# Performance work log

Measured on AMD Instinct MI355X. Metric: run time of the kernel, lower is better.

The kernel has to match this reference:

```python
import jax, jax.numpy as jnp
import numpy as np

N = 8192
TAU = 0.5
B = 4096


def _factorize(n, tau):
    # Precompute LU factorization of the tridiagonal implicit-Laplace matrix,
    # mirroring the torch __init__ exactly.
    b = np.full(n - 1, -tau, dtype=np.float32)   # upper diagonal
    a = np.full(n, 1.0 + 2.0 * tau, dtype=np.float32)  # main diagonal
    c = np.full(n - 1, -tau, dtype=np.float32)   # lower diagonal
    a[0] = 1.0 + tau
    a[-1] = 1.0 + tau
    for i in range(n - 1):
        c[i] = c[i] / a[i]
        a[i + 1] = a[i + 1] - c[i] * b[i]
    return a, b, c


def setup_inputs() -> dict:
    key = jax.random.key(0)
    a, b, c = _factorize(N, TAU)
    x = jax.random.normal(key, (B, N), dtype=jnp.float32)
    return {
        "x": x,
        "a": jnp.asarray(a),
        "b": jnp.asarray(b),
        "c": jnp.asarray(c),
    }


def reference(x, a, b, c):
    # Thomas algorithm with precomputed LU factors.
    # Forward substitution:  y[0] = x[0];  y[i] = x[i] - y[i-1] * c[i-1]
    # Back substitution:     z[N-1] = y[N-1] / a[N-1];
    #                        z[i]   = (y[i] - z[i+1] * b[i]) / a[i]
    xt = x.T  # [N, B] so the scan runs over the grid axis
    c_pad = jnp.concatenate([jnp.zeros((1,), x.dtype), c])  # c_pad[0]=0 -> y[0]=x[0]

    def fwd_step(y_prev, inp):
        xi, ci = inp
        yi = xi - y_prev * ci
        return yi, yi

    _, y = jax.lax.scan(fwd_step, jnp.zeros_like(xt[0]), (xt, c_pad))

    b_pad = jnp.concatenate([b, jnp.zeros((1,), x.dtype)])  # b_pad[N-1]=0

    def bwd_step(z_next, inp):
        yi, bi, ai = inp
        zi = (yi - z_next * bi) / ai
        return zi, zi

    _, z = jax.lax.scan(bwd_step, jnp.zeros_like(y[0]), (y, b_pad, a), reverse=True)
    return z.T  # [B, N]
```

## Files before the change

kernel.cpp:

```cpp
#include <hip/hip_runtime.h>


#define NN    8192
#define BB    4096
#define CHUNK 128
#define HALO  32
#define WIN   (CHUNK + HALO)

__device__ __forceinline__ float fast_rcp(float v) {
#if defined(__has_builtin) && __has_builtin(__builtin_amdgcn_rcpf)
    float r = __builtin_amdgcn_rcpf(v);
    r = r * (2.0f - v * r);
    return r;
#else
    return 1.0f / v;
#endif
}

template<bool FIRST, bool EDGE>
__device__ __forceinline__ void solve_window(
    const float* __restrict__ xrow,
    const float* __restrict__ a,
    const float* __restrict__ b,
    const float* __restrict__ c,
    float* __restrict__ orow,
    int s)
{
    const float* xs = xrow + s;
    const float* as = a + s;
    const float* bs = b + s;
    const float* cs = c + s;

    float y = 0.0f;

    if (!FIRST) {
        const float* xw = xrow + (s - HALO);
        const float* cw = c + (s - HALO);
        #pragma unroll
        for (int k = 0; k < HALO; k += 4) {
            float4 xv = *(const float4*)(xw + k);
            y = xv.x - cw[k - 1] * y;
            y = xv.y - cw[k]     * y;
            y = xv.z - cw[k + 1] * y;
            y = xv.w - cw[k + 2] * y;
        }
    }

    float ybuf[WIN];
    #pragma unroll
    for (int k = 0; k < (EDGE ? CHUNK : WIN); k += 4) {
        float4 xv = *(const float4*)(xs + k);
        float c0 = (FIRST && k == 0) ? 0.0f : cs[k - 1];
        y = xv.x - c0        * y;  ybuf[k]     = y;
        y = xv.y - cs[k]     * y;  ybuf[k + 1] = y;
        y = xv.z - cs[k + 1] * y;  ybuf[k + 2] = y;
        y = xv.w - cs[k + 2] * y;  ybuf[k + 3] = y;
    }

    float z = 0.0f;
    if (!EDGE) {
        #pragma unroll
        for (int k = WIN - 1; k >= CHUNK; --k) {
            z = (ybuf[k] - bs[k] * z) * fast_rcp(as[k]);
        }
        #pragma unroll
        for (int kg = CHUNK - 4; kg >= 0; kg -= 4) {
            float4 zv;
            z = (ybuf[kg + 3] - bs[kg + 3] * z) * fast_rcp(as[kg + 3]); zv.w = z;
            z = (ybuf[kg + 2] - bs[kg + 2] * z) * fast_rcp(as[kg + 2]); zv.z = z;
            z = (ybuf[kg + 1] - bs[kg + 1] * z) * fast_rcp(as[kg + 1]); zv.y = z;
            z = (ybuf[kg]     - bs[kg]     * z) * fast_rcp(as[kg]);     zv.x = z;
            *(float4*)(orow + s + kg) = zv;
        }
    } else {
        {
            float4 zv;
            z = ybuf[CHUNK - 1] * fast_rcp(as[CHUNK - 1]);                          zv.w = z;
            z = (ybuf[CHUNK - 2] - bs[CHUNK - 2] * z) * fast_rcp(as[CHUNK - 2]);    zv.z = z;
            z = (ybuf[CHUNK - 3] - bs[CHUNK - 3] * z) * fast_rcp(as[CHUNK - 3]);    zv.y = z;
            z = (ybuf[CHUNK - 4] - bs[CHUNK - 4] * z) * fast_rcp(as[CHUNK - 4]);    zv.x = z;
            *(float4*)(orow + s + CHUNK - 4) = zv;
        }
        #pragma unroll
        for (int kg = CHUNK - 8; kg >= 0; kg -= 4) {
            float4 zv;
            z = (ybuf[kg + 3] - bs[kg + 3] * z) * fast_rcp(as[kg + 3]); zv.w = z;
            z = (ybuf[kg + 2] - bs[kg + 2] * z) * fast_rcp(as[kg + 2]); zv.z = z;
            z = (ybuf[kg + 1] - bs[kg + 1] * z) * fast_rcp(as[kg + 1]); zv.y = z;
            z = (ybuf[kg]     - bs[kg]     * z) * fast_rcp(as[kg]);     zv.x = z;
            *(float4*)(orow + s + kg) = zv;
        }
    }
}

__global__ __launch_bounds__(256, 2) void TriDiagonalLaplaceSolver_kernel(
    const float* __restrict__ x,
    const float* __restrict__ a,
    const float* __restrict__ b,
    const float* __restrict__ c,
    float* __restrict__ out)
{
    const int chunk = blockIdx.x;
    const int row   = blockIdx.y * 256 + threadIdx.x;
    const int s     = chunk * CHUNK;

    const float* xrow = x   + (size_t)row * NN;
    float*       orow = out + (size_t)row * NN;

    if (chunk == 0) {
        solve_window<true, false>(xrow, a, b, c, orow, 0);
    } else if (chunk == (NN / CHUNK) - 1) {
        solve_window<false, true>(xrow, a, b, c, orow, s);
    } else {
        solve_window<false, false>(xrow, a, b, c, orow, s);
    }
}

extern "C" void kernel_launch(void* const* d_in, const int* in_sizes, int n_in,
                              void* d_out, int out_size, void* d_ws, size_t ws_size,
                              hipStream_t stream) {
    const float* x = (const float*)d_in[0];
    const float* a = (const float*)d_in[1];
    const float* b = (const float*)d_in[2];
    const float* c = (const float*)d_in[3];
    float* out = (float*)d_out;

    dim3 grid(NN / CHUNK, BB / 256);
    dim3 block(256);
    TriDiagonalLaplaceSolver_kernel<<<grid, block, 0, stream>>>(x, a, b, c, out);
}
```

Before: 316.3 us.

## Halve chunk size, raise occupancy, and defer output stores until after back-substitution

Shrinks each thread's chunk from 128 to 64 elements and raises the launch-bounds minimum from 2 to 4 blocks per CU, so the smaller register buffer allows more waves in flight. Back-substitution now writes results into the register buffer, and all float4 stores happen in a final loop instead of being interleaved with the recurrence. The cost is more redundant halo work, since 32 extra elements per 64 outputs is a larger share than before, and more grid blocks. The preprocessor fallback around the rcp builtin is also removed.

```diff
diff --git a/kernel.cpp b/kernel.cpp
--- a/kernel.cpp
+++ b/kernel.cpp
@@ -3,18 +3,14 @@
 
 #define NN    8192
 #define BB    4096
-#define CHUNK 128
+#define CHUNK 64
 #define HALO  32
 #define WIN   (CHUNK + HALO)
 
 __device__ __forceinline__ float fast_rcp(float v) {
-#if defined(__has_builtin) && __has_builtin(__builtin_amdgcn_rcpf)
     float r = __builtin_amdgcn_rcpf(v);
     r = r * (2.0f - v * r);
     return r;
-#else
-    return 1.0f / v;
-#endif
 }
 
 template<bool FIRST, bool EDGE>
@@ -64,36 +60,32 @@
             z = (ybuf[k] - bs[k] * z) * fast_rcp(as[k]);
         }
         #pragma unroll
-        for (int kg = CHUNK - 4; kg >= 0; kg -= 4) {
-            float4 zv;
-            z = (ybuf[kg + 3] - bs[kg + 3] * z) * fast_rcp(as[kg + 3]); zv.w = z;
-            z = (ybuf[kg + 2] - bs[kg + 2] * z) * fast_rcp(as[kg + 2]); zv.z = z;
-            z = (ybuf[kg + 1] - bs[kg + 1] * z) * fast_rcp(as[kg + 1]); zv.y = z;
-            z = (ybuf[kg]     - bs[kg]     * z) * fast_rcp(as[kg]);     zv.x = z;
-            *(float4*)(orow + s + kg) = zv;
+        for (int k = CHUNK - 1; k >= 0; --k) {
+            z = (ybuf[k] - bs[k] * z) * fast_rcp(as[k]);
+            ybuf[k] = z;
         }
     } else {
-        {
-            float4 zv;
-            z = ybuf[CHUNK - 1] * fast_rcp(as[CHUNK - 1]);                          zv.w = z;
-            z = (ybuf[CHUNK - 2] - bs[CHUNK - 2] * z) * fast_rcp(as[CHUNK - 2]);    zv.z = z;
-            z = (ybuf[CHUNK - 3] - bs[CHUNK - 3] * z) * fast_rcp(as[CHUNK - 3]);    zv.y = z;
-            z = (ybuf[CHUNK - 4] - bs[CHUNK - 4] * z) * fast_rcp(as[CHUNK - 4]);    zv.x = z;
-            *(float4*)(orow + s + CHUNK - 4) = zv;
+        z = ybuf[CHUNK - 1] * fast_rcp(as[CHUNK - 1]);
+        ybuf[CHUNK - 1] = z;
+        #pragma unroll
+        for (int k = CHUNK - 2; k >= 0; --k) {
+            z = (ybuf[k] - bs[k] * z) * fast_rcp(as[k]);
+            ybuf[k] = z;
         }
-        #pragma unroll
-        for (int kg = CHUNK - 8; kg >= 0; kg -= 4) {
-            float4 zv;
-            z = (ybuf[kg + 3] - bs[kg + 3] * z) * fast_rcp(as[kg + 3]); zv.w = z;
-            z = (ybuf[kg + 2] - bs[kg + 2] * z) * fast_rcp(as[kg + 2]); zv.z = z;
-            z = (ybuf[kg + 1] - bs[kg + 1] * z) * fast_rcp(as[kg + 1]); zv.y = z;
-            z = (ybuf[kg]     - bs[kg]     * z) * fast_rcp(as[kg]);     zv.x = z;
-            *(float4*)(orow + s + kg) = zv;
-        }
+    }
+
+    #pragma unroll
+    for (int k = 0; k < CHUNK; k += 4) {
+        float4 zv;
+        zv.x = ybuf[k];
+        zv.y = ybuf[k + 1];
+        zv.z = ybuf[k + 2];
+        zv.w = ybuf[k + 3];
+        *(float4*)(orow + s + k) = zv;
     }
 }
 
-__global__ __launch_bounds__(256, 2) void TriDiagonalLaplaceSolver_kernel(
+__global__ __launch_bounds__(256, 4) void TriDiagonalLaplaceSolver_kernel(
     const float* __restrict__ x,
     const float* __restrict__ a,
     const float* __restrict__ b,
```

New measurement: 337.7 us. 6.8% more time.
